# Kernel tuning notes

Measured on AMD Instinct MI355X. Metric: run time of the kernel, lower is better.

The kernel has to match this reference:

```python
import jax, jax.numpy as jnp
import numpy as np

# ---- model hyperparameters (match init_kwargs) ----
N_ATOMS = 16000
N_EDGES = 256000
F = 128          # n_atom_basis
NF = 32          # n_filters
L = 3            # n_interactions
N_RBF = 20
CUTOFF = 5.0
MAX_Z = 100
INV_SQRT_F = np.float32(1.0 / np.sqrt(F))
INV_SQRT_2NF = np.float32(1.0 / np.sqrt(2 * NF))
SQ2 = np.float32(np.sqrt(2.0)); SQ3 = np.float32(np.sqrt(3.0)); SQ6 = np.float32(np.sqrt(6.0))
LOG2 = np.float32(np.log(2.0))


def ssp(x):
    # shifted softplus: softplus(x) - log(2)
    return jax.nn.softplus(x) - LOG2


def setup_inputs() -> dict:
    key = jax.random.key(0)
    k = jax.random.split(key, 16)
    Z = jax.random.randint(k[0], (N_ATOMS,), 0, MAX_Z)
    r_ij = jax.random.normal(k[1], (N_EDGES, 3), dtype=jnp.float32) * 2.0
    idx_i = jnp.sort(jax.random.randint(k[2], (N_EDGES,), 0, N_ATOMS))
    idx_j = jax.random.randint(k[3], (N_EDGES,), 0, N_ATOMS)
    # parameters (e3nn Linear: N(0,1) weights with explicit 1/sqrt(fan_in) in the math;
    # filter-network Dense: fan-in scaled weights, zero bias; padding_idx=0 -> zero row)
    emb = jax.random.normal(k[4], (MAX_Z, F), dtype=jnp.float32).at[0].set(0.0)
    W_pe = jax.random.normal(k[5], (F, F), dtype=jnp.float32)
    W0s = jax.random.normal(k[6], (L, F, NF), dtype=jnp.float32)   # in2f, 0e path
    W0v = jax.random.normal(k[7], (L, F, NF), dtype=jnp.float32)   # in2f, 1o path
    Wf1 = jax.random.normal(k[8], (L, N_RBF, NF), dtype=jnp.float32) / np.sqrt(N_RBF)
    bf1 = jnp.zeros((L, NF), jnp.float32)
    Wf2 = jax.random.normal(k[9], (L, NF, 6 * NF), dtype=jnp.float32) / np.sqrt(NF)
    bf2 = jnp.zeros((L, 6 * NF), jnp.float32)
    As = jax.random.normal(k[10], (L, 2 * NF, F), dtype=jnp.float32)  # f2out_1 0e
    Av = jax.random.normal(k[11], (L, 2 * NF, F), dtype=jnp.float32)  # f2out_1 1o
    Bs = jax.random.normal(k[12], (L, F, F), dtype=jnp.float32)       # f2out_2 0e
    Bv = jax.random.normal(k[13], (L, F, F), dtype=jnp.float32)       # f2out_2 1o
    return dict(Z=Z, r_ij=r_ij, idx_i=idx_i, idx_j=idx_j, emb=emb, W_pe=W_pe,
                W0s=W0s, W0v=W0v, Wf1=Wf1, bf1=bf1, Wf2=Wf2, bf2=bf2,
                As=As, Av=Av, Bs=Bs, Bv=Bv)


def _interaction(xs, xv, idx_i, idx_j, f_ij, rcut, Yv,
                 W0s, W0v, Wf1, bf1, Wf2, bf2, As, Av, Bs, Bv):
    n_atoms = xs.shape[0]
    # in2f: e3nn o3.Linear (per-l channel mixing, fan-in normalized)
    hs = (xs @ W0s) * INV_SQRT_F                        # [N, NF]  (0e)
    hv = jnp.einsum('nfc,fg->ngc', xv, W0v) * INV_SQRT_F  # [N, NF, 3] (1o)
    sj = hs[idx_j]                                      # gather neighbors [E, NF]
    vj = hv[idx_j]                                      # [E, NF, 3]
    # FullTensorProduct (0e+1o) x Y(0e+1o); Y0 = 1, Y1 = sqrt(3)*r_hat (component norm)
    Yb = Yv[:, None, :]                                 # [E, 1, 3]
    t0a = sj                                            # 0e x 0e -> 0e
    t0b = jnp.einsum('efc,ec->ef', vj, Yv) / SQ3        # 1o x 1o -> 0e
    t1a = sj[:, :, None] * Yb                           # 0e x 1o -> 1o
    t1b = vj                                            # 1o x 0e -> 1o
    t1e = jnp.cross(vj, Yb) / SQ2                       # 1o x 1o -> 1e
    ux, uy, uz = vj[..., 0], vj[..., 1], vj[..., 2]
    wx, wy, wz = Yv[:, None, 0], Yv[:, None, 1], Yv[:, None, 2]
    t2e = jnp.stack([(ux * wy + uy * wx) / SQ2,         # 1o x 1o -> 2e (sym traceless)
                     (uy * wz + uz * wy) / SQ2,
                     (2 * uz * wz - ux * wx - uy * wy) / SQ6,
                     (ux * wz + uz * wx) / SQ2,
                     (ux * wx - uy * wy) / SQ2], axis=-1)  # [E, NF, 5]
    # filter network + cutoff envelope: W_ij [E, 6*NF] (one scalar per irrep)
    W = (ssp(f_ij @ Wf1 + bf1) @ Wf2 + bf2) * rcut[:, None]
    w0a, w0b, w1a, w1b, w1e, w2e = jnp.split(W, 6, axis=1)
    E = sj.shape[0]
    # elementwise tensor product (scale each irrep by its scalar), then scatter-add
    y_all = jnp.concatenate([
        t0a * w0a, t0b * w0b,
        (t1a * w1a[..., None]).reshape(E, -1),
        (t1b * w1b[..., None]).reshape(E, -1),
        (t1e * w1e[..., None]).reshape(E, -1),
        (t2e * w2e[..., None]).reshape(E, -1)], axis=1)   # [E, 16*NF]
    agg = jax.ops.segment_sum(y_all, idx_i, num_segments=n_atoms)  # [N, 16*NF]
    s_in = agg[:, :2 * NF]
    v_in = agg[:, 2 * NF:8 * NF].reshape(n_atoms, 2 * NF, 3)
    # f2out_1: output irreps are F x (0e+1o) -> 1e and 2e channels have no path (dropped)
    os = ssp((s_in @ As) * INV_SQRT_2NF)                # f2out_1 + scalar activation
    ov = jnp.einsum('nfc,fg->ngc', v_in, Av) * INV_SQRT_2NF
    os = (os @ Bs) * INV_SQRT_F                         # f2out_2
    ov = jnp.einsum('nfc,fg->ngc', ov, Bv) * INV_SQRT_F
    return os, ov


def _forward(Z, r_ij, idx_i, idx_j, emb, W_pe, W0s, W0v, Wf1, bf1, Wf2, bf2, As, Av, Bs, Bv):
    xs = (emb[Z] @ W_pe) * INV_SQRT_F                   # embedding + post_embedding (0e)
    xv = jnp.zeros((xs.shape[0], F, 3), xs.dtype)       # 1o part starts at zero (no 0e->1o path)
    d = jnp.linalg.norm(r_ij, axis=1)
    offsets = jnp.linspace(0.0, CUTOFF, N_RBF).astype(jnp.float32)
    coeff = -0.5 / (offsets[1] - offsets[0]) ** 2
    f_ij = jnp.exp(coeff * (d[:, None] - offsets) ** 2)  # Gaussian RBF [E, N_RBF]
    rcut = 0.5 * (jnp.cos(np.float32(np.pi) * d / CUTOFF) + 1.0) * (d < CUTOFF)
    # spherical harmonics, normalize=True + component normalization (Y0=1, Y1=sqrt(3)*rhat);
    # the r_ij*rcut prescaling in the original doesn't change the direction, and edges with
    # rcut=0 contribute nothing since W_ij carries the rcut factor.
    Yv = SQ3 * r_ij / jnp.maximum(d, 1e-9)[:, None]
    for l in range(L):
        vs, vv = _interaction(xs, xv, idx_i, idx_j, f_ij, rcut, Yv,
                              W0s[l], W0v[l], Wf1[l], bf1[l], Wf2[l], bf2[l],
                              As[l], Av[l], Bs[l], Bv[l])
        xs = xs + vs
        xv = xv + vv
    return xs  # scalar_representation [N, F]


def reference(Z, r_ij, idx_i, idx_j, emb, W_pe, W0s, W0v, Wf1, bf1, Wf2, bf2, As, Av, Bs, Bv):
    return _forward(Z, r_ij, idx_i, idx_j, emb, W_pe, W0s, W0v, Wf1, bf1, Wf2, bf2, As, Av, Bs, Bv)
```

## Files before the change

kernel.cpp:

```cpp
#include <hip/hip_runtime.h>
#include <math.h>

constexpr int NA   = 16000;
constexpr int NE   = 256000;
constexpr int F    = 128;
constexpr int NF   = 32;
constexpr int NRBF = 20;
constexpr float CUTOFF       = 5.0f;
constexpr float INV_SQRT_F   = 0.0883883476483184f;
constexpr float INV_SQRT_2NF = 0.125f;
constexpr float INV_SQ3      = 0.5773502691896258f;
constexpr float SQ3          = 1.7320508075688772f;
constexpr float LOG2_        = 0.6931471805599453f;
constexpr float PI_          = 3.14159265358979323f;

typedef _Float16 h2 __attribute__((ext_vector_type(2)));

__device__ __forceinline__ float ssp(float x) {
    return fmaxf(x, 0.0f) + __logf(1.0f + __expf(-fabsf(x))) - LOG2_;
}
__device__ __forceinline__ float fdot2(h2 a, h2 b, float c) {
#if __has_builtin(__builtin_amdgcn_fdot2)
    return __builtin_amdgcn_fdot2(a, b, c, false);
#else
    return c + (float)a[0]*(float)b[0] + (float)a[1]*(float)b[1];
#endif
}

__global__ void geom_kernel(const float* __restrict__ r_ij,
                            float* __restrict__ fijT,
                            float* __restrict__ yvrT) {
    int e = blockIdx.x * blockDim.x + threadIdx.x;
    if (e >= NE) return;
    float x = r_ij[3*e+0], y = r_ij[3*e+1], z = r_ij[3*e+2];
    float d = sqrtf(x*x + y*y + z*z);
    const float delta = CUTOFF / (NRBF - 1);
    const float coeff = -0.5f / (delta * delta);
    #pragma unroll
    for (int k = 0; k < NRBF; k++) {
        float t = d - delta * (float)k;
        fijT[(size_t)k*NE + e] = __expf(coeff * t * t);
    }
    float rc = 0.5f * (__cosf(PI_ * d / CUTOFF) + 1.0f);
    rc = (d < CUTOFF) ? rc : 0.0f;
    float inv = SQ3 / fmaxf(d, 1e-9f);
    yvrT[0*(size_t)NE + e] = x * inv;
    yvrT[1*(size_t)NE + e] = y * inv;
    yvrT[2*(size_t)NE + e] = z * inv;
    yvrT[3*(size_t)NE + e] = rc;
}

__global__ void preph_kernel(const float* __restrict__ Wf2, const float* __restrict__ Wf1,
                             h2* __restrict__ Wf2H, h2* __restrict__ Wf1H) {
    int u = blockIdx.x * 256 + threadIdx.x;
    if (u < 3*128*16) {
        int l = u / (128*16), rem = u % (128*16), c = rem >> 4, k2 = rem & 15;
        const float* W = Wf2 + (size_t)l*NF*192;
        Wf2H[u] = h2{(_Float16)W[(2*k2)*192 + c], (_Float16)W[(2*k2+1)*192 + c]};
    }
    if (u < 3*320) {
        int l = u / 320, rem = u % 320, k2 = rem >> 5, g = rem & 31;
        const float* W = Wf1 + (size_t)l*NRBF*NF;
        Wf1H[u] = h2{(_Float16)W[(2*k2)*32 + g], (_Float16)W[(2*k2+1)*32 + g]};
    }
}

__global__ void prep2_kernel(const float* __restrict__ Av, const float* __restrict__ Bv,
                             float* __restrict__ AvBv) {
    int u = blockIdx.x * 256 + threadIdx.x;
    if (u >= 3*64*128) return;
    int l = u >> 13, rem = u & 8191, f = rem >> 7, c = rem & 127;
    const float* av = Av + (size_t)l*64*128 + f*128;
    const float* bv = Bv + (size_t)l*128*128 + c;
    float acc = 0.f;
    #pragma unroll 8
    for (int g = 0; g < 128; g++) acc += av[g] * bv[(size_t)g*128];
    AvBv[u] = acc * (INV_SQRT_2NF * INV_SQRT_F);
}

__global__ __launch_bounds__(256, 4)
void embed_kernel(const int* __restrict__ Z,
                  const float* __restrict__ emb,
                  const float* __restrict__ Wpe,
                  const float* __restrict__ W0s,
                  float* __restrict__ xs,
                  float* __restrict__ hsv) {
    __shared__ float ER[32][128];
    __shared__ int   Zs[32];
    int t = threadIdx.x;
    int a0 = blockIdx.x * 32;
    if (t < 32) Zs[t] = Z[a0 + t];
    __syncthreads();
    {
        const float4* emb4 = (const float4*)emb;
        float4* ER4 = (float4*)&ER[0][0];
        #pragma unroll
        for (int it = 0; it < 4; it++) {
            int u4 = it*256 + t;
            int a = u4 >> 5, k4 = u4 & 31;
            ER4[u4] = emb4[(size_t)Zs[a]*32 + k4];
        }
    }
    __syncthreads();
    int c = t & 127, half = t >> 7;
    float acc[16];
    #pragma unroll
    for (int a = 0; a < 16; a++) acc[a] = 0.f;
    for (int k = 0; k < 128; k++) {
        float w = Wpe[k*128 + c];
        #pragma unroll
        for (int a = 0; a < 16; a++) acc[a] += ER[half*16 + a][k] * w;
    }
    __syncthreads();
    #pragma unroll
    for (int a = 0; a < 16; a++) {
        float v = acc[a] * INV_SQRT_F;
        xs[(size_t)(a0 + half*16 + a)*128 + c] = v;
        ER[half*16 + a][c] = v;
    }
    __syncthreads();
    {
        int g = t & 31, rr = t >> 5;
        float a2[4] = {0.f, 0.f, 0.f, 0.f};
        for (int k = 0; k < 128; k++) {
            float w = W0s[k*32 + g];
            #pragma unroll
            for (int a = 0; a < 4; a++) a2[a] += ER[rr*4 + a][k] * w;
        }
        #pragma unroll
        for (int a = 0; a < 4; a++)
            hsv[(size_t)(a0 + rr*4 + a)*128 + g] = a2[a] * INV_SQRT_F;
        for (int u = t; u < 32*96; u += 256) {
            int a = u / 96, rem = u - a*96;
            hsv[(size_t)(a0 + a)*128 + 32 + rem] = 0.f;
        }
    }
}

struct alignas(16) HRow { h2 v[20]; };

template <bool DO_V>
__global__ __launch_bounds__(256, 4)
void agg_kernel(const int* __restrict__ idx_i,
                const int* __restrict__ idx_j,
                const float* __restrict__ fijT,
                const float* __restrict__ yvrT,
                const float* __restrict__ hsv,
                const h2* __restrict__ Wf1H,
                const float* __restrict__ bf1,
                const h2* __restrict__ Wf2H,
                const float* __restrict__ bf2,
                float* __restrict__ aggG) {
    __shared__ h2 LW1[320];
    __shared__ HRow HB[4][64];
    int t = threadIdx.x;
    for (int u = t; u < 320; u += 256) LW1[u] = Wf1H[u];
    __syncthreads();

    int wid = t >> 6, lane = t & 63;
    int base = (blockIdx.x*4 + wid) * 64;

    int   il = idx_i[base + lane];
    int   jl = idx_j[base + lane];
    float y0l = yvrT[0*(size_t)NE + base + lane];
    float y1l = yvrT[1*(size_t)NE + base + lane];
    float y2l = yvrT[2*(size_t)NE + base + lane];
    float y3l = yvrT[3*(size_t)NE + base + lane];

    int ilp = __shfl_up(il, 1);
    unsigned long long bmask = __ballot(lane > 0 && il != ilp);

    h2 fp[10];
    #pragma unroll
    for (int k2 = 0; k2 < 10; k2++) {
        float fa = fijT[(size_t)(2*k2)*NE + base + lane];
        float fb = fijT[(size_t)(2*k2+1)*NE + base + lane];
        fp[k2] = h2{(_Float16)fa, (_Float16)fb};
    }
    float h[32];
    #pragma unroll
    for (int g = 0; g < 32; g++) h[g] = bf1[g];
    #pragma unroll
    for (int k2 = 0; k2 < 10; k2++) {
        #pragma unroll
        for (int g = 0; g < 32; g++)
            h[g] = fdot2(fp[k2], LW1[k2*32 + g], h[g]);
    }
    #pragma unroll
    for (int g = 0; g < 32; g++) h[g] = ssp(h[g]);
    {
        h2 hp[16];
        #pragma unroll
        for (int i = 0; i < 16; i++) hp[i] = h2{(_Float16)h[2*i], (_Float16)h[2*i+1]};
        float4* dst = (float4*)HB[wid][lane].v;
        const float4* srcp = (const float4*)hp;
        #pragma unroll
        for (int w = 0; w < 4; w++) dst[w] = srcp[w];
    }

    h2 w2a[16], w2b[16];
    #pragma unroll
    for (int k2 = 0; k2 < 16; k2++) w2a[k2] = Wf2H[lane*16 + k2];
    if (DO_V) {
        #pragma unroll
        for (int k2 = 0; k2 < 16; k2++) w2b[k2] = Wf2H[(64+lane)*16 + k2];
    }
    float bf2a = bf2[lane];
    float bf2b = DO_V ? bf2[64 + lane] : 0.f;

    int idxQ = 32 + 3*(lane - 32);

    float a0 = 0.f, a1 = 0.f, a2 = 0.f, a3 = 0.f;
    int prev = __builtin_amdgcn_readlane(il, 0);

    for (int ii = 0; ii < 64; ++ii) {
        if ((bmask >> ii) & 1ull) {
            unsafeAtomicAdd(&aggG[(size_t)prev*256 + lane], a0);
            a0 = 0.f;
            if (DO_V) {
                unsafeAtomicAdd(&aggG[(size_t)prev*256 + 64 + lane],  a1);
                unsafeAtomicAdd(&aggG[(size_t)prev*256 + 128 + lane], a2);
                unsafeAtomicAdd(&aggG[(size_t)prev*256 + 192 + lane], a3);
                a1 = a2 = a3 = 0.f;
            }
            prev = __builtin_amdgcn_readlane(il, ii);
        }
        int j = __builtin_amdgcn_readlane(jl, ii);
        const float* row = hsv + (size_t)j*128;
        float q0, q1, q2;
        if (lane < 32) {
            q0 = row[lane]; q1 = q0; q2 = q0;
        } else {
            const float* p = row + idxQ;
            q0 = p[0]; q1 = p[1]; q2 = p[2];
        }
        float s0 = bf2a, s1 = bf2b;
        {
            const float4* hq4 = (const float4*)HB[wid][ii].v;
            float4 bb[4];
            bb[0] = hq4[0]; bb[1] = hq4[1]; bb[2] = hq4[2]; bb[3] = hq4[3];
            const h2* hh = (const h2*)bb;
            #pragma unroll
            for (int k2 = 0; k2 < 16; k2++) {
                s0 = fdot2(hh[k2], w2a[k2], s0);
                if (DO_V) s1 = fdot2(hh[k2], w2b[k2], s1);
            }
        }
        float y3s = __int_as_float(__builtin_amdgcn_readlane(__float_as_int(y3l), ii));
        float y0s = __int_as_float(__builtin_amdgcn_readlane(__float_as_int(y0l), ii));
        float y1s = __int_as_float(__builtin_amdgcn_readlane(__float_as_int(y1l), ii));
        float y2s = __int_as_float(__builtin_amdgcn_readlane(__float_as_int(y2l), ii));
        float w0 = s0 * y3s;
        float dot = (q0*y0s + q1*y1s + q2*y2s) * INV_SQ3;
        float v0 = (lane < 32) ? q0 : dot;
        a0 += v0 * w0;
        if (DO_V) {
            float w1 = s1 * y3s;
            float m1 = (lane < 32) ? y0s : 1.0f;
            float m2 = (lane < 32) ? y1s : 1.0f;
            float m3 = (lane < 32) ? y2s : 1.0f;
            a1 += q0 * m1 * w1;
            a2 += q1 * m2 * w1;
            a3 += q2 * m3 * w1;
        }
    }
    unsafeAtomicAdd(&aggG[(size_t)prev*256 + lane], a0);
    if (DO_V) {
        unsafeAtomicAdd(&aggG[(size_t)prev*256 + 64 + lane],  a1);
        unsafeAtomicAdd(&aggG[(size_t)prev*256 + 128 + lane], a2);
        unsafeAtomicAdd(&aggG[(size_t)prev*256 + 192 + lane], a3);
    }
}

template <bool DO_V, bool XV_WRITE, bool MAKE_H>
__global__ __launch_bounds__(256, 3)
void mlp_kernel(const float* __restrict__ aggG,
                const float* __restrict__ As,
                const float* __restrict__ Bs,
                const float* __restrict__ AvBv,
                const float* __restrict__ W0sN,
                const float* __restrict__ W0vN,
                float* __restrict__ xs,
                float* __restrict__ xv,
                float* __restrict__ hsv) {
    constexpr int AC  = DO_V ? 256 : 64;
    constexpr int XR  = MAKE_H ? 16 : 1;
    constexpr int XC  = MAKE_H ? 384 : 1;
    __shared__ float aggL[16][AC];
    __shared__ float outL[16][128];
    __shared__ float xvL[XR][XC];
    int t = threadIdx.x;
    int a0 = blockIdx.x * 16;
    {
        const float4* g4 = (const float4*)(aggG + (size_t)a0*256);
        if (DO_V) {
            float4* l4 = (float4*)&aggL[0][0];
            #pragma unroll
            for (int it = 0; it < 4; it++) l4[it*256 + t] = g4[it*256 + t];
        } else {
            int row = t >> 4, c4 = t & 15;
            *(float4*)&aggL[row][c4*4] = g4[row*64 + c4];
        }
    }
    __syncthreads();

    int q  = t & 31;
    int rp = t >> 5;
    const float4* As4 = (const float4*)As;
    const float4* Bs4 = (const float4*)Bs;

    {
        float ox0=0,oy0=0,oz0=0,ow0=0, ox1=0,oy1=0,oz1=0,ow1=0;
        const float4* x0p = (const float4*)&aggL[rp][0];
        const float4* x1p = (const float4*)&aggL[rp+8][0];
        #pragma unroll 4
        for (int kq = 0; kq < 16; kq++) {
            float4 x0 = x0p[kq], x1 = x1p[kq];
            float4 wa = As4[(4*kq+0)*32 + q];
            float4 wb = As4[(4*kq+1)*32 + q];
            float4 wc = As4[(4*kq+2)*32 + q];
            float4 wd = As4[(4*kq+3)*32 + q];
            ox0 += x0.x*wa.x + x0.y*wb.x + x0.z*wc.x + x0.w*wd.x;
            oy0 += x0.x*wa.y + x0.y*wb.y + x0.z*wc.y + x0.w*wd.y;
            oz0 += x0.x*wa.z + x0.y*wb.z + x0.z*wc.z + x0.w*wd.z;
            ow0 += x0.x*wa.w + x0.y*wb.w + x0.z*wc.w + x0.w*wd.w;
            ox1 += x1.x*wa.x + x1.y*wb.x + x1.z*wc.x + x1.w*wd.x;
            oy1 += x1.x*wa.y + x1.y*wb.y + x1.z*wc.y + x1.w*wd.y;
            oz1 += x1.x*wa.z + x1.y*wb.z + x1.z*wc.z + x1.w*wd.z;
            ow1 += x1.x*wa.w + x1.y*wb.w + x1.z*wc.w + x1.w*wd.w;
        }
        float4 r0 = { ssp(ox0*INV_SQRT_2NF), ssp(oy0*INV_SQRT_2NF), ssp(oz0*INV_SQRT_2NF), ssp(ow0*INV_SQRT_2NF) };
        float4 r1 = { ssp(ox1*INV_SQRT_2NF), ssp(oy1*INV_SQRT_2NF), ssp(oz1*INV_SQRT_2NF), ssp(ow1*INV_SQRT_2NF) };
        *(float4*)&outL[rp][4*q]   = r0;
        *(float4*)&outL[rp+8][4*q] = r1;
    }
    if (DO_V) {
        const float4* AB4 = (const float4*)AvBv;
        int ra[6], rc[6];
        #pragma unroll
        for (int i = 0; i < 6; i++) {
            int rv = rp + 8*i;
            ra[i] = rv/3; rc[i] = rv - 3*(rv/3);
        }
        float o[6][4];
        #pragma unroll
        for (int i = 0; i < 6; i++) { o[i][0]=0; o[i][1]=0; o[i][2]=0; o[i][3]=0; }
        const float4* vp[6];
        #pragma unroll
        for (int i = 0; i < 6; i++)
            vp[i] = (const float4*)&aggL[ra[i]][64 + rc[i]*64];
        #pragma unroll 2
        for (int kq = 0; kq < 16; kq++) {
            float4 wa = AB4[(4*kq+0)*32 + q];
            float4 wb = AB4[(4*kq+1)*32 + q];
            float4 wc = AB4[(4*kq+2)*32 + q];
            float4 wd = AB4[(4*kq+3)*32 + q];
            #pragma unroll
            for (int i = 0; i < 6; i++) {
                float4 x = vp[i][kq];
                o[i][0] += x.x*wa.x + x.y*wb.x + x.z*wc.x + x.w*wd.x;
                o[i][1] += x.x*wa.y + x.y*wb.y + x.z*wc.y + x.w*wd.y;
                o[i][2] += x.x*wa.z + x.y*wb.z + x.z*wc.z + x.w*wd.z;
                o[i][3] += x.x*wa.w + x.y*wb.w + x.z*wc.w + x.w*wd.w;
            }
        }
        #pragma unroll
        for (int i = 0; i < 6; i++) {
            float4* p = (float4*)&xv[(size_t)(a0+ra[i])*384 + rc[i]*128 + 4*q];
            float4 c;
            if (XV_WRITE) {
                c = make_float4(o[i][0], o[i][1], o[i][2], o[i][3]);
            } else {
                c = *p;
                c.x += o[i][0]; c.y += o[i][1]; c.z += o[i][2]; c.w += o[i][3];
            }
            *p = c;
            if (MAKE_H) *(float4*)&xvL[ra[i]][rc[i]*128 + 4*q] = c;
        }
    }
    __syncthreads();
    {
        float ox0=0,oy0=0,oz0=0,ow0=0, ox1=0,oy1=0,oz1=0,ow1=0;
        const float4* x0p = (const float4*)&outL[rp][0];
        const float4* x1p = (const float4*)&outL[rp+8][0];
        #pragma unroll 4
        for (int kq = 0; kq < 32; kq++) {
            float4 x0 = x0p[kq], x1 = x1p[kq];
            float4 wa = Bs4[(4*kq+0)*32 + q];
            float4 wb = Bs4[(4*kq+1)*32 + q];
            float4 wc = Bs4[(4*kq+2)*32 + q];
            float4 wd = Bs4[(4*kq+3)*32 + q];
            ox0 += x0.x*wa.x + x0.y*wb.x + x0.z*wc.x + x0.w*wd.x;
            oy0 += x0.x*wa.y + x0.y*wb.y + x0.z*wc.y + x0.w*wd.y;
            oz0 += x0.x*wa.z + x0.y*wb.z + x0.z*wc.z + x0.w*wd.z;
            ow0 += x0.x*wa.w + x0.y*wb.w + x0.z*wc.w + x0.w*wd.w;
            ox1 += x1.x*wa.x + x1.y*wb.x + x1.z*wc.x + x1.w*wd.x;
            oy1 += x1.x*wa.y + x1.y*wb.y + x1.z*wc.y + x1.w*wd.y;
            oz1 += x1.x*wa.z + x1.y*wb.z + x1.z*wc.z + x1.w*wd.z;
            ow1 += x1.x*wa.w + x1.y*wb.w + x1.z*wc.w + x1.w*wd.w;
        }
        float4* p0 = (float4*)&xs[(size_t)(a0+rp)*128 + 4*q];
        float4* p1 = (float4*)&xs[(size_t)(a0+rp+8)*128 + 4*q];
        float4 c0 = *p0, c1 = *p1;
        c0.x += ox0*INV_SQRT_F; c0.y += oy0*INV_SQRT_F; c0.z += oz0*INV_SQRT_F; c0.w += ow0*INV_SQRT_F;
        c1.x += ox1*INV_SQRT_F; c1.y += oy1*INV_SQRT_F; c1.z += oz1*INV_SQRT_F; c1.w += ow1*INV_SQRT_F;
        *p0 = c0; *p1 = c1;
        if (MAKE_H) {
            *(float4*)&aggL[rp][4*q]   = c0;
            *(float4*)&aggL[rp+8][4*q] = c1;
        }
    }
    if (MAKE_H) {
        __syncthreads();
        int g = t & 31, r = t >> 5;
        int sel = r & 3, half = r >> 2;
        const float* W = (sel == 0) ? W0sN : W0vN;
        const float* src;
        int stride;
        if (sel == 0) { src = &aggL[half*8][0];              stride = AC; }
        else          { src = &xvL[half*8][(sel-1)*128];     stride = XC; }
        float acc[8];
        #pragma unroll
        for (int a = 0; a < 8; a++) acc[a] = 0.f;
        for (int k = 0; k < 128; k++) {
            float w = W[k*32 + g];
            #pragma unroll
            for (int a = 0; a < 8; a++) acc[a] += src[a*stride + k] * w;
        }
        #pragma unroll
        for (int a = 0; a < 8; a++) {
            int n = a0 + half*8 + a;
            if (sel == 0) hsv[(size_t)n*128 + g] = acc[a] * INV_SQRT_F;
            else          hsv[(size_t)n*128 + 32 + g*3 + (sel-1)] = acc[a] * INV_SQRT_F;
        }
    }
}

extern "C" void kernel_launch(void* const* d_in, const int* in_sizes, int n_in,
                              void* d_out, int out_size, void* d_ws, size_t ws_size,
                              hipStream_t stream) {
    (void)in_sizes; (void)n_in; (void)out_size; (void)ws_size;
    const int*   Z     = (const int*)  d_in[0];
    const float* r_ij  = (const float*)d_in[1];
    const int*   idx_i = (const int*)  d_in[2];
    const int*   idx_j = (const int*)  d_in[3];
    const float* emb   = (const float*)d_in[4];
    const float* Wpe   = (const float*)d_in[5];
    const float* W0s   = (const float*)d_in[6];
    const float* W0v   = (const float*)d_in[7];
    const float* Wf1   = (const float*)d_in[8];
    const float* bf1   = (const float*)d_in[9];
    const float* Wf2   = (const float*)d_in[10];
    const float* bf2   = (const float*)d_in[11];
    const float* As    = (const float*)d_in[12];
    const float* Av    = (const float*)d_in[13];
    const float* Bs    = (const float*)d_in[14];
    const float* Bv    = (const float*)d_in[15];

    float* xs = (float*)d_out;
    float* ws = (float*)d_ws;
    float* fijT = ws;
    float* yvrT = fijT + (size_t)NE*NRBF;
    float* xv   = yvrT + (size_t)NE*4;
    float* hsv  = xv   + (size_t)NA*F*3;
    float* aggG = hsv  + (size_t)NA*F;
    float* AvBv = aggG + (size_t)NA*256;
    h2*    Wf2H = (h2*)(AvBv + (size_t)3*64*128);
    h2*    Wf1H = Wf2H + (size_t)3*128*16;

    geom_kernel<<<(NE+255)/256, 256, 0, stream>>>(r_ij, fijT, yvrT);
    preph_kernel<<<24, 256, 0, stream>>>(Wf2, Wf1, Wf2H, Wf1H);
    prep2_kernel<<<(3*64*128+255)/256, 256, 0, stream>>>(Av, Bv, AvBv);
    embed_kernel<<<NA/32, 256, 0, stream>>>(Z, emb, Wpe, W0s, xs, hsv);

    for (int l = 0; l < 3; l++) {
        hipMemsetAsync(aggG, 0, (size_t)NA*256*sizeof(float), stream);

        if (l < 2)
            agg_kernel<true><<<NE/256, 256, 0, stream>>>(idx_i, idx_j, fijT, yvrT, hsv,
                Wf1H + (size_t)l*320, bf1 + (size_t)l*NF,
                Wf2H + (size_t)l*128*16, bf2 + (size_t)l*6*NF, aggG);
        else
            agg_kernel<false><<<NE/256, 256, 0, stream>>>(idx_i, idx_j, fijT, yvrT, hsv,
                Wf1H + (size_t)l*320, bf1 + (size_t)l*NF,
                Wf2H + (size_t)l*128*16, bf2 + (size_t)l*6*NF, aggG);

        if (l == 0)
            mlp_kernel<true, true, true><<<NA/16, 256, 0, stream>>>(aggG,
                As + (size_t)l*2*NF*F, Bs + (size_t)l*F*F, AvBv + (size_t)l*64*128,
                W0s + (size_t)(l+1)*F*NF, W0v + (size_t)(l+1)*F*NF, xs, xv, hsv);
        else if (l == 1)
            mlp_kernel<true, false, true><<<NA/16, 256, 0, stream>>>(aggG,
                As + (size_t)l*2*NF*F, Bs + (size_t)l*F*F, AvBv + (size_t)l*64*128,
                W0s + (size_t)(l+1)*F*NF, W0v + (size_t)(l+1)*F*NF, xs, xv, hsv);
        else
            mlp_kernel<false, false, false><<<NA/16, 256, 0, stream>>>(aggG,
                As + (size_t)l*2*NF*F, Bs + (size_t)l*F*F, AvBv + (size_t)l*64*128,
                W0s, W0v, xs, xv, hsv);
    }
}
```

Baseline: 402.8 us.

## Split h projection into separate kernel, fuse agg zeroing, prefetch edge rows

The per-atom projection that produces hsv moves out of the MLP kernel into a standalone h_kernel launched before each aggregation. This lets the MLP kernel drop its extra shared buffers and raise occupancy (launch bounds 3 to 4), and it now zeroes aggG after reading it, replacing the per-layer memset. The aggregation loop software-prefetches the next edge's hsv row and HB fp16 vector one iteration ahead, and pins the Wf2 weights in registers with empty asm. The costs are an extra kernel launch per layer, a re-read of xs and xv from global memory, and higher register pressure in the aggregation loop.

Measured after the change: 357.4 us, median of 3. 11.3% less time.

```diff
diff --git a/kernel.cpp b/kernel.cpp
--- a/kernel.cpp
+++ b/kernel.cpp
@@ -134,6 +134,53 @@
             int a = u / 96, rem = u - a*96;
             hsv[(size_t)(a0 + a)*128 + 32 + rem] = 0.f;
         }
+    }
+}
+
+__global__ __launch_bounds__(256, 4)
+void h_kernel(const float* __restrict__ xs,
+              const float* __restrict__ xv,
+              const float* __restrict__ W0s,
+              const float* __restrict__ W0v,
+              float* __restrict__ hsv) {
+    __shared__ float X[16][512];
+    int t = threadIdx.x;
+    int a0 = blockIdx.x * 16;
+    {
+        float* Xf = &X[0][0];
+        const float4* xs4 = (const float4*)xs;
+        const float4* xv4 = (const float4*)xv;
+        #pragma unroll
+        for (int it = 0; it < 2; it++) {
+            int u4 = it*256 + t;
+            int a = u4 >> 5, k4 = u4 & 31;
+            *(float4*)&Xf[a*512 + k4*4] = xs4[(size_t)a0*32 + u4];
+        }
+        #pragma unroll
+        for (int it = 0; it < 6; it++) {
+            int u4 = it*256 + t;
+            int a = u4 / 96, rem = u4 - a*96;
+            *(float4*)&Xf[a*512 + 128 + rem*4] = xv4[(size_t)a0*96 + u4];
+        }
+    }
+    __syncthreads();
+    int g = t & 31, r = t >> 5;
+    int sel = r & 3, half = r >> 2;
+    const float* W = (sel == 0) ? W0s : W0v;
+    int xoff = (sel == 0) ? 0 : (128 + (sel-1)*128);
+    float acc[8];
+    #pragma unroll
+    for (int a = 0; a < 8; a++) acc[a] = 0.f;
+    for (int k = 0; k < 128; k++) {
+        float w = W[k*32 + g];
+        #pragma unroll
+        for (int a = 0; a < 8; a++) acc[a] += X[half*8 + a][xoff + k] * w;
+    }
+    #pragma unroll
+    for (int a = 0; a < 8; a++) {
+        int n = a0 + half*8 + a;
+        if (sel == 0) hsv[(size_t)n*128 + g] = acc[a] * INV_SQRT_F;
+        else          hsv[(size_t)n*128 + 32 + g*3 + (sel-1)] = acc[a] * INV_SQRT_F;
     }
 }
 
@@ -200,20 +247,47 @@
 
     h2 w2a[16], w2b[16];
     #pragma unroll
-    for (int k2 = 0; k2 < 16; k2++) w2a[k2] = Wf2H[lane*16 + k2];
+    for (int k2 = 0; k2 < 16; k2++) {
+        w2a[k2] = Wf2H[lane*16 + k2];
+        asm volatile("" : "+v"(w2a[k2]));
+    }
     if (DO_V) {
         #pragma unroll
-        for (int k2 = 0; k2 < 16; k2++) w2b[k2] = Wf2H[(64+lane)*16 + k2];
+        for (int k2 = 0; k2 < 16; k2++) {
+            w2b[k2] = Wf2H[(64+lane)*16 + k2];
+            asm volatile("" : "+v"(w2b[k2]));
+        }
     }
     float bf2a = bf2[lane];
     float bf2b = DO_V ? bf2[64 + lane] : 0.f;
 
     int idxQ = 32 + 3*(lane - 32);
+    int off0 = (lane < 32) ? lane : idxQ;
+    int off1 = (lane < 32) ? lane : (idxQ + 1);
+    int off2 = (lane < 32) ? lane : (idxQ + 2);
 
     float a0 = 0.f, a1 = 0.f, a2 = 0.f, a3 = 0.f;
     int prev = __builtin_amdgcn_readlane(il, 0);
 
+    float qn0, qn1, qn2;
+    float4 hbn[4];
+    {
+        int j = __builtin_amdgcn_readlane(jl, 0);
+        const float* row = hsv + (size_t)j*128;
+        qn0 = row[off0]; qn1 = row[off1]; qn2 = row[off2];
+        const float4* hq4 = (const float4*)HB[wid][0].v;
+        hbn[0] = hq4[0]; hbn[1] = hq4[1]; hbn[2] = hq4[2]; hbn[3] = hq4[3];
+    }
     for (int ii = 0; ii < 64; ++ii) {
+        float q0 = qn0, q1 = qn1, q2 = qn2;
+        float4 hbc[4] = { hbn[0], hbn[1], hbn[2], hbn[3] };
+        if (ii < 63) {
+            int j = __builtin_amdgcn_readlane(jl, ii + 1);
+            const float* row = hsv + (size_t)j*128;
+            qn0 = row[off0]; qn1 = row[off1]; qn2 = row[off2];
+            const float4* hq4 = (const float4*)HB[wid][ii + 1].v;
+            hbn[0] = hq4[0]; hbn[1] = hq4[1]; hbn[2] = hq4[2]; hbn[3] = hq4[3];
+        }
         if ((bmask >> ii) & 1ull) {
             unsafeAtomicAdd(&aggG[(size_t)prev*256 + lane], a0);
             a0 = 0.f;
@@ -225,21 +299,9 @@
             }
             prev = __builtin_amdgcn_readlane(il, ii);
         }
-        int j = __builtin_amdgcn_readlane(jl, ii);
-        const float* row = hsv + (size_t)j*128;
-        float q0, q1, q2;
-        if (lane < 32) {
-            q0 = row[lane]; q1 = q0; q2 = q0;
-        } else {
-            const float* p = row + idxQ;
-            q0 = p[0]; q1 = p[1]; q2 = p[2];
-        }
         float s0 = bf2a, s1 = bf2b;
         {
-            const float4* hq4 = (const float4*)HB[wid][ii].v;
-            float4 bb[4];
-            bb[0] = hq4[0]; bb[1] = hq4[1]; bb[2] = hq4[2]; bb[3] = hq4[3];
-            const h2* hh = (const h2*)bb;
+            const h2* hh = (const h2*)hbc;
             #pragma unroll
             for (int k2 = 0; k2 < 16; k2++) {
                 s0 = fdot2(hh[k2], w2a[k2], s0);
@@ -272,23 +334,18 @@
     }
 }
 
-template <bool DO_V, bool XV_WRITE, bool MAKE_H>
-__global__ __launch_bounds__(256, 3)
+template <bool DO_V, bool XV_WRITE, bool ZERO_AGG>
+__global__ __launch_bounds__(256, 4)
 void mlp_kernel(const float* __restrict__ aggG,
                 const float* __restrict__ As,
                 const float* __restrict__ Bs,
                 const float* __restrict__ AvBv,
-                const float* __restrict__ W0sN,
-                const float* __restrict__ W0vN,
                 float* __restrict__ xs,
                 float* __restrict__ xv,
-                float* __restrict__ hsv) {
-    constexpr int AC  = DO_V ? 256 : 64;
-    constexpr int XR  = MAKE_H ? 16 : 1;
-    constexpr int XC  = MAKE_H ? 384 : 1;
+                float* __restrict__ aggW) {
+    constexpr int AC = DO_V ? 256 : 64;
     __shared__ float aggL[16][AC];
     __shared__ float outL[16][128];
-    __shared__ float xvL[XR][XC];
     int t = threadIdx.x;
     int a0 = blockIdx.x * 16;
     {
@@ -303,6 +360,12 @@
         }
     }
     __syncthreads();
+    if (ZERO_AGG) {
+        float4 z = make_float4(0.f, 0.f, 0.f, 0.f);
+        float4* g4w = (float4*)(aggW + (size_t)a0*256);
+        #pragma unroll
+        for (int it = 0; it < 4; it++) g4w[it*256 + t] = z;
+    }
 
     int q  = t & 31;
     int rp = t >> 5;
@@ -367,15 +430,14 @@
         #pragma unroll
         for (int i = 0; i < 6; i++) {
             float4* p = (float4*)&xv[(size_t)(a0+ra[i])*384 + rc[i]*128 + 4*q];
-            float4 c;
             if (XV_WRITE) {
-                c = make_float4(o[i][0], o[i][1], o[i][2], o[i][3]);
+                float4 c = make_float4(o[i][0], o[i][1], o[i][2], o[i][3]);
+                *p = c;
             } else {
-                c = *p;
+                float4 c = *p;
                 c.x += o[i][0]; c.y += o[i][1]; c.z += o[i][2]; c.w += o[i][3];
+                *p = c;
             }
-            *p = c;
-            if (MAKE_H) *(float4*)&xvL[ra[i]][rc[i]*128 + 4*q] = c;
         }
     }
     __syncthreads();
@@ -405,34 +467,6 @@
         c0.x += ox0*INV_SQRT_F; c0.y += oy0*INV_SQRT_F; c0.z += oz0*INV_SQRT_F; c0.w += ow0*INV_SQRT_F;
         c1.x += ox1*INV_SQRT_F; c1.y += oy1*INV_SQRT_F; c1.z += oz1*INV_SQRT_F; c1.w += ow1*INV_SQRT_F;
         *p0 = c0; *p1 = c1;
-        if (MAKE_H) {
-            *(float4*)&aggL[rp][4*q]   = c0;
-            *(float4*)&aggL[rp+8][4*q] = c1;
-        }
-    }
-    if (MAKE_H) {
-        __syncthreads();
-        int g = t & 31, r = t >> 5;
-        int sel = r & 3, half = r >> 2;
-        const float* W = (sel == 0) ? W0sN : W0vN;
-        const float* src;
-        int stride;
-        if (sel == 0) { src = &aggL[half*8][0];              stride = AC; }
-        else          { src = &xvL[half*8][(sel-1)*128];     stride = XC; }
-        float acc[8];
-        #pragma unroll
-        for (int a = 0; a < 8; a++) acc[a] = 0.f;
-        for (int k = 0; k < 128; k++) {
-            float w = W[k*32 + g];
-            #pragma unroll
-            for (int a = 0; a < 8; a++) acc[a] += src[a*stride + k] * w;
-        }
-        #pragma unroll
-        for (int a = 0; a < 8; a++) {
-            int n = a0 + half*8 + a;
-            if (sel == 0) hsv[(size_t)n*128 + g] = acc[a] * INV_SQRT_F;
-            else          hsv[(size_t)n*128 + 32 + g*3 + (sel-1)] = acc[a] * INV_SQRT_F;
-        }
     }
 }
 
@@ -472,9 +506,12 @@
     preph_kernel<<<24, 256, 0, stream>>>(Wf2, Wf1, Wf2H, Wf1H);
     prep2_kernel<<<(3*64*128+255)/256, 256, 0, stream>>>(Av, Bv, AvBv);
     embed_kernel<<<NA/32, 256, 0, stream>>>(Z, emb, Wpe, W0s, xs, hsv);
+    hipMemsetAsync(aggG, 0, (size_t)NA*256*sizeof(float), stream);
 
     for (int l = 0; l < 3; l++) {
-        hipMemsetAsync(aggG, 0, (size_t)NA*256*sizeof(float), stream);
+        if (l > 0)
+            h_kernel<<<NA/16, 256, 0, stream>>>(xs, xv,
+                W0s + (size_t)l*F*NF, W0v + (size_t)l*F*NF, hsv);
 
         if (l < 2)
             agg_kernel<true><<<NE/256, 256, 0, stream>>>(idx_i, idx_j, fijT, yvrT, hsv,
@@ -488,14 +525,14 @@
         if (l == 0)
             mlp_kernel<true, true, true><<<NA/16, 256, 0, stream>>>(aggG,
                 As + (size_t)l*2*NF*F, Bs + (size_t)l*F*F, AvBv + (size_t)l*64*128,
-                W0s + (size_t)(l+1)*F*NF, W0v + (size_t)(l+1)*F*NF, xs, xv, hsv);
+                xs, xv, aggG);
         else if (l == 1)
             mlp_kernel<true, false, true><<<NA/16, 256, 0, stream>>>(aggG,
                 As + (size_t)l*2*NF*F, Bs + (size_t)l*F*F, AvBv + (size_t)l*64*128,
-                W0s + (size_t)(l+1)*F*NF, W0v + (size_t)(l+1)*F*NF, xs, xv, hsv);
+                xs, xv, aggG);
         else
             mlp_kernel<false, false, false><<<NA/16, 256, 0, stream>>>(aggG,
                 As + (size_t)l*2*NF*F, Bs + (size_t)l*F*F, AvBv + (size_t)l*64*128,
-                W0s, W0v, xs, xv, hsv);
-    }
-}
+                xs, xv, aggG);
+    }
+}
```
